# Performance work log

Hardware: AMD Instinct MI355X
Metric: run time of the kernel (lower is better)

## Reference

```python
import jax, jax.numpy as jnp
import numpy as np

NUM_GROUPS = 32
EPS = 1e-5
HEADS = 8
DIM_HEAD = 64


def group_norm(x, w, b):
    # x: [B, C, L]; normalize over (C/G, L) per group
    B, C, L = x.shape
    xg = x.reshape(B, NUM_GROUPS, C // NUM_GROUPS, L)
    mu = jnp.mean(xg, axis=(2, 3), keepdims=True)
    var = jnp.var(xg, axis=(2, 3), keepdims=True)
    xn = ((xg - mu) * jax.lax.rsqrt(var + EPS)).reshape(B, C, L)
    return xn * w[None, :, None] + b[None, :, None]


def setup_inputs() -> dict:
    key = jax.random.key(0)
    k1, k2, k3 = jax.random.split(key, 3)
    dim, hidden = 512, HEADS * DIM_HEAD
    B, L = 4, 2048
    x = jax.random.normal(k1, (B, dim, L), dtype=jnp.float32)
    gn_w = jnp.ones((dim,), jnp.float32)
    gn_b = jnp.zeros((dim,), jnp.float32)
    w_qkv = jax.random.normal(k2, (3 * hidden, dim), jnp.float32) * (dim ** -0.5)
    w_out = jax.random.normal(k3, (dim, hidden), jnp.float32) * (hidden ** -0.5)
    b_out = jnp.zeros((dim,), jnp.float32)
    return {"x": x, "gn_w": gn_w, "gn_b": gn_b, "w_qkv": w_qkv, "w_out": w_out, "b_out": b_out}


def reference(x, gn_w, gn_b, w_qkv, w_out, b_out):
    B, C, L = x.shape
    scale = DIM_HEAD ** -0.5
    nx = group_norm(x, gn_w, gn_b)
    # 1x1 conv == channel matmul: [3H*D, C] x [B, C, L] -> [B, 3H*D, L]
    qkv = jnp.einsum('oc,bcl->bol', w_qkv, nx)
    q, k, v = jnp.split(qkv, 3, axis=1)
    rs = lambda t: t.reshape(B, HEADS, DIM_HEAD, L)
    q, k, v = rs(q) * scale, rs(k), rs(v)
    sim = jnp.einsum('bhdi,bhdj->bhij', q, k)         # [B,H,L,L]
    attn = jax.nn.softmax(sim, axis=-1)
    out = jnp.einsum('bhij,bhdj->bhdi', attn, v)       # [B,H,D,L]
    out = out.reshape(B, HEADS * DIM_HEAD, L)
    proj = jnp.einsum('oc,bcl->bol', w_out, out) + b_out[None, :, None]
    return proj + x
```

## Files before the change

kernel.cpp:

```cpp
#include <hip/hip_runtime.h>

#define DEVI __device__ __forceinline__

typedef unsigned short u16;
typedef unsigned int u32;
typedef __attribute__((ext_vector_type(8))) __bf16 bf16x8;
typedef __attribute__((ext_vector_type(2))) __bf16 bf16x2;
typedef __attribute__((ext_vector_type(4))) float f32x4;
typedef __attribute__((ext_vector_type(16))) float f32x16;
typedef __attribute__((ext_vector_type(4))) u32 u32x4;

DEVI u16 f2bf(float f){
  u32 u = __float_as_uint(f);
  return (u16)((u + 0x7FFFu + ((u >> 16) & 1u)) >> 16);
}
DEVI u32 pk2(float lo, float hi){
  bf16x2 t; t[0] = (__bf16)lo; t[1] = (__bf16)hi;
  return __builtin_bit_cast(u32, t);
}

__global__ __launch_bounds__(256) void gnstat_kernel(const float* __restrict__ x,
                                                     float2* __restrict__ pstat){
  int bg = blockIdx.x >> 2, qt = blockIdx.x & 3;
  const float4* xin = (const float4*)(x + (size_t)bg*32768 + qt*8192);
  int tid = threadIdx.x;
  float s1 = 0.f, s2 = 0.f;
  #pragma unroll
  for (int i = 0; i < 8; ++i){
    float4 v = xin[tid + i*256];
    s1 += v.x + v.y + v.z + v.w;
    s2 += v.x*v.x + v.y*v.y + v.z*v.z + v.w*v.w;
  }
  __shared__ float red[8];
  int lane = tid & 63, w = tid >> 6;
  for (int off = 32; off; off >>= 1){
    s1 += __shfl_down(s1, off);
    s2 += __shfl_down(s2, off);
  }
  if (lane == 0){ red[w] = s1; red[4 + w] = s2; }
  __syncthreads();
  if (tid == 0){
    pstat[blockIdx.x] = make_float2(red[0]+red[1]+red[2]+red[3],
                                    red[4]+red[5]+red[6]+red[7]);
  }
}

__global__ __launch_bounds__(128) void gnfin_kernel(const float2* __restrict__ pstat,
                                                    float2* __restrict__ stat){
  int t = threadIdx.x;
  float s1 = 0.f, s2 = 0.f;
  #pragma unroll
  for (int i = 0; i < 4; ++i){
    float2 p = pstat[t*4 + i];
    s1 += p.x; s2 += p.y;
  }
  float mu = s1 * (1.f/32768.f);
  float var = s2 * (1.f/32768.f) - mu*mu;
  stat[t] = make_float2(mu, rsqrtf(var + 1e-5f));
}

__global__ __launch_bounds__(256) void normtrans_kernel(const float* __restrict__ x,
                                                        const float2* __restrict__ stat,
                                                        const float* __restrict__ gw,
                                                        const float* __restrict__ gb,
                                                        u16* __restrict__ nxT){
  int b = blockIdx.z, c0 = blockIdx.y * 64, l0 = blockIdx.x * 64;
  __shared__ u16 T[64][72];
  int tid = threadIdx.x;
  #pragma unroll
  for (int rep = 0; rep < 2; ++rep){
    int task = tid + rep*256;
    int r = task >> 3, cc = task & 7;
    int ch = c0 + r;
    float2 st = stat[b*32 + (ch >> 4)];
    float ga = gw[ch] * st.y;
    float be = gb[ch] - st.x * ga;
    const float4* src = (const float4*)(x + ((size_t)(b*512 + ch))*2048 + l0 + cc*8);
    float4 v0 = src[0], v1 = src[1];
    ushort4 o0, o1;
    o0.x = f2bf(v0.x*ga + be); o0.y = f2bf(v0.y*ga + be);
    o0.z = f2bf(v0.z*ga + be); o0.w = f2bf(v0.w*ga + be);
    o1.x = f2bf(v1.x*ga + be); o1.y = f2bf(v1.y*ga + be);
    o1.z = f2bf(v1.z*ga + be); o1.w = f2bf(v1.w*ga + be);
    *(ushort4*)&T[r][cc*8]     = o0;
    *(ushort4*)&T[r][cc*8 + 4] = o1;
  }
  __syncthreads();
  #pragma unroll
  for (int rep = 0; rep < 2; ++rep){
    int task = tid + rep*256;
    int r = task >> 3, cc = task & 7;
    u16 tmp[8];
    #pragma unroll
    for (int i = 0; i < 8; ++i) tmp[i] = T[cc*8 + i][r];
    *(uint4*)(nxT + ((size_t)(b*2048 + l0 + r))*512 + c0 + cc*8) = *(uint4*)tmp;
  }
}

__global__ __launch_bounds__(256) void castw_kernel(const float* __restrict__ wq,
                                                    const float* __restrict__ wo,
                                                    u16* __restrict__ wqb,
                                                    u16* __restrict__ wob){
  int t = blockIdx.x * 256 + threadIdx.x;
  const int NQ4 = (1536*512)/4;
  float4 v; u16* dst;
  if (t < NQ4){ v = ((const float4*)wq)[t]; dst = wqb + t*4; }
  else        { int u_ = t - NQ4; v = ((const float4*)wo)[u_]; dst = wob + u_*4; }
  ushort4 s;
  s.x = f2bf(v.x); s.y = f2bf(v.y); s.z = f2bf(v.z); s.w = f2bf(v.w);
  *(ushort4*)dst = s;
}

template<int MODE>
__global__ __launch_bounds__(256) void gemm_kernel(const u16* __restrict__ A,
                                                   const u16* __restrict__ Bm,
                                                   u16* __restrict__ q_o,
                                                   u16* __restrict__ k_o,
                                                   u16* __restrict__ v_o,
                                                   const float* __restrict__ bo,
                                                   const float* __restrict__ xres,
                                                   float* __restrict__ out){
  int b  = blockIdx.z;
  int n0 = blockIdx.x * 128, m0 = blockIdx.y * 128;
  int tid = threadIdx.x, w = tid >> 6, lane = tid & 63, lq = lane >> 4, lr = lane & 15;
  int wm = (w >> 1) * 64, wn = (w & 1) * 64;
  __shared__ u16 Al[2][128][40], Bl[2][128][40];
  f32x4 acc[4][4] = {};
  const u16* Bb = Bm + (size_t)b * 2048 * 512;

  for (int k0 = 0; k0 < 512; k0 += 64){
    #pragma unroll
    for (int rep = 0; rep < 4; ++rep){
      int task = tid + rep*256;
      int row = task >> 3, kc = task & 7;
      *(uint4*)&Al[kc>>2][row][(kc&3)*8] = *(const uint4*)(A  + (size_t)(m0+row)*512 + k0 + kc*8);
      *(uint4*)&Bl[kc>>2][row][(kc&3)*8] = *(const uint4*)(Bb + (size_t)(n0+row)*512 + k0 + kc*8);
    }
    __syncthreads();
    #pragma unroll
    for (int half = 0; half < 2; ++half){
      bf16x8 af[4], bfr[4];
      #pragma unroll
      for (int i = 0; i < 4; ++i) af[i]  = *(const bf16x8*)&Al[half][wm + i*16 + lr][lq*8];
      #pragma unroll
      for (int j = 0; j < 4; ++j) bfr[j] = *(const bf16x8*)&Bl[half][wn + j*16 + lr][lq*8];
      #pragma unroll
      for (int i = 0; i < 4; ++i)
        #pragma unroll
        for (int j = 0; j < 4; ++j)
          acc[i][j] = __builtin_amdgcn_mfma_f32_16x16x32_bf16(af[i], bfr[j], acc[i][j], 0, 0, 0);
    }
    __syncthreads();
  }

  if (MODE == 0){
    const float QSCALE = 0.125f * 1.4426950408889634f;
    #pragma unroll
    for (int i = 0; i < 4; ++i){
      int o0  = m0 + wm + i*16 + lq*4;
      int cls = o0 >> 9;
      int hh  = (o0 >> 6) & 7;
      int d0  = o0 & 63;
      size_t hbase = (size_t)(b*8+hh) * 2048 * 64;
      #pragma unroll
      for (int j = 0; j < 4; ++j){
        int l = n0 + wn + j*16 + lr;
        f32x4 v = acc[i][j];
        if (cls == 0){
          ushort4 s;
          s.x = f2bf(v[0]*QSCALE); s.y = f2bf(v[1]*QSCALE);
          s.z = f2bf(v[2]*QSCALE); s.w = f2bf(v[3]*QSCALE);
          *(ushort4*)(q_o + hbase + (size_t)l*64 + d0) = s;
        } else if (cls == 1){
          size_t off = (size_t)(((l>>5)*4 + (d0>>4)))*512
                     + ((d0>>3)&1)*256 + (l&31)*8 + (d0&7);
          ushort4 s;
          s.x = f2bf(v[0]); s.y = f2bf(v[1]); s.z = f2bf(v[2]); s.w = f2bf(v[3]);
          *(ushort4*)(k_o + hbase + off) = s;
        } else {
          size_t off = (size_t)(((l>>4)*2 + (d0>>5)))*512
                     + ((l>>3)&1)*256 + (l&7);
          #pragma unroll
          for (int r = 0; r < 4; ++r)
            v_o[hbase + off + ((d0+r)&31)*8] = f2bf(v[r]);
        }
      }
    }
  } else {
    #pragma unroll
    for (int i = 0; i < 4; ++i){
      int o0 = m0 + wm + i*16 + lq*4;
      #pragma unroll
      for (int j = 0; j < 4; ++j){
        int l = n0 + wn + j*16 + lr;
        #pragma unroll
        for (int r = 0; r < 4; ++r){
          int o = o0 + r;
          size_t idx = ((size_t)b*512 + o)*2048 + l;
          out[idx] = acc[i][j][r] + bo[o] + xres[idx];
        }
      }
    }
  }
}

__global__ __launch_bounds__(256, 2) void attn_kernel(const u16* __restrict__ qT,
                                                      const u16* __restrict__ kF,
                                                      const u16* __restrict__ vF,
                                                      u16* __restrict__ ao){
  int flat = blockIdx.x;
  int xcd = flat & 7, tt = flat >> 3;
  int bh = xcd*4 + (tt & 3);
  int qb = tt >> 2;
  int tid = threadIdx.x, w = tid >> 6, l = tid & 63;
  int l31 = l & 31, h = l >> 5;
  int q0 = qb*128 + w*32;
  size_t hoff = (size_t)bh * 2048 * 64;

  const u16* qp = qT + hoff + (size_t)(q0 + l31)*64 + 8*h;
  bf16x8 qf0 = *(const bf16x8*)(qp);
  bf16x8 qf1 = *(const bf16x8*)(qp + 16);
  bf16x8 qf2 = *(const bf16x8*)(qp + 32);
  bf16x8 qf3 = *(const bf16x8*)(qp + 48);

  const u16* kbase = kF + hoff + (size_t)l*8;
  const u16* vbase = vF + hoff + (size_t)l*8;

  f32x16 o0 = {}, o1 = {};
  float m = -1e30f, lsum = 0.f;

  bf16x8 kA0,kA1,kA2,kA3, kB0,kB1,kB2,kB3;
  bf16x8 vA0,vA1,vA2,vA3, vB0,vB1,vB2,vB3;
  f32x16 sA, sB;
  bf16x8 Bf0, Bf1;

#define LDK(P, t) { const u16* kt_ = kbase + (t)*2048;                         \
    P##0 = *(const bf16x8*)(kt_);        P##1 = *(const bf16x8*)(kt_ + 512);   \
    P##2 = *(const bf16x8*)(kt_ + 1024); P##3 = *(const bf16x8*)(kt_ + 1536); }
#define LDV(P, t) { const u16* vt_ = vbase + (t)*2048;                         \
    P##0 = *(const bf16x8*)(vt_);        P##1 = *(const bf16x8*)(vt_ + 512);   \
    P##2 = *(const bf16x8*)(vt_ + 1024); P##3 = *(const bf16x8*)(vt_ + 1536); }
#define QKT(S, P) {                                                            \
    S = (f32x16){};                                                            \
    __builtin_amdgcn_s_setprio(1);                                             \
    S = __builtin_amdgcn_mfma_f32_32x32x16_bf16(P##0, qf0, S, 0, 0, 0);        \
    S = __builtin_amdgcn_mfma_f32_32x32x16_bf16(P##1, qf1, S, 0, 0, 0);        \
    S = __builtin_amdgcn_mfma_f32_32x32x16_bf16(P##2, qf2, S, 0, 0, 0);        \
    S = __builtin_amdgcn_mfma_f32_32x32x16_bf16(P##3, qf3, S, 0, 0, 0);        \
    __builtin_amdgcn_s_setprio(0); }
#define SMAX(S) { \
    float c0 = fmaxf(S[0],S[1]),  c1 = fmaxf(S[2],S[3]);                       \
    float c2 = fmaxf(S[4],S[5]),  c3 = fmaxf(S[6],S[7]);                       \
    float c4 = fmaxf(S[8],S[9]),  c5 = fmaxf(S[10],S[11]);                     \
    float c6 = fmaxf(S[12],S[13]),c7 = fmaxf(S[14],S[15]);                     \
    c0 = fmaxf(c0,c1); c2 = fmaxf(c2,c3); c4 = fmaxf(c4,c5); c6 = fmaxf(c6,c7);\
    c0 = fmaxf(c0,c2); c4 = fmaxf(c4,c6); c0 = fmaxf(c0,c4);                   \
    c0 = fmaxf(c0, __shfl_xor(c0, 32));                                        \
    if (__any(c0 > m + 8.f)){                                                  \
      float nm = fmaxf(m, c0);                                                 \
      float alpha = __builtin_amdgcn_exp2f(m - nm);                            \
      m = nm; lsum *= alpha;                                                   \
      _Pragma("unroll")                                                        \
      for (int i = 0; i < 16; ++i){ o0[i] *= alpha; o1[i] *= alpha; }          \
    }                                                                          \
    float p[16];                                                               \
    _Pragma("unroll")                                                          \
    for (int i = 0; i < 16; ++i) p[i] = __builtin_amdgcn_exp2f(S[i] - m);      \
    float t0 = p[0]+p[1],  t1 = p[2]+p[3],  t2 = p[4]+p[5],  t3 = p[6]+p[7];   \
    float t4 = p[8]+p[9],  t5 = p[10]+p[11],t6 = p[12]+p[13],t7 = p[14]+p[15]; \
    t0 += t1; t2 += t3; t4 += t5; t6 += t7; t0 += t2; t4 += t6; t0 += t4;      \
    lsum += t0 + __shfl_xor(t0, 32);                                           \
    u32 a0 = pk2(p[0],p[1]),   a1 = pk2(p[2],p[3]);                            \
    u32 a2 = pk2(p[4],p[5]),   a3 = pk2(p[6],p[7]);                            \
    u32 a4 = pk2(p[8],p[9]),   a5 = pk2(p[10],p[11]);                          \
    u32 a6 = pk2(p[12],p[13]), a7 = pk2(p[14],p[15]);                          \
    u32 x0 = __shfl_xor((int)a0,32), x1 = __shfl_xor((int)a1,32);              \
    u32 x2 = __shfl_xor((int)a2,32), x3 = __shfl_xor((int)a3,32);              \
    u32 x4 = __shfl_xor((int)a4,32), x5 = __shfl_xor((int)a5,32);              \
    u32 x6 = __shfl_xor((int)a6,32), x7 = __shfl_xor((int)a7,32);              \
    u32x4 wb0, wb1;                                                            \
    wb0[0] = h ? x2 : a0;  wb0[1] = h ? x3 : a1;                               \
    wb0[2] = h ? a2 : x0;  wb0[3] = h ? a3 : x1;                               \
    wb1[0] = h ? x6 : a4;  wb1[1] = h ? x7 : a5;                               \
    wb1[2] = h ? a6 : x4;  wb1[3] = h ? a7 : x5;                               \
    Bf0 = __builtin_bit_cast(bf16x8, wb0);                                     \
    Bf1 = __builtin_bit_cast(bf16x8, wb1); }
#define PVA(P) {                                                               \
    __builtin_amdgcn_s_setprio(1);                                             \
    o0 = __builtin_amdgcn_mfma_f32_32x32x16_bf16(P##0, Bf0, o0, 0, 0, 0);      \
    o1 = __builtin_amdgcn_mfma_f32_32x32x16_bf16(P##1, Bf0, o1, 0, 0, 0);      \
    o0 = __builtin_amdgcn_mfma_f32_32x32x16_bf16(P##2, Bf1, o0, 0, 0, 0);      \
    o1 = __builtin_amdgcn_mfma_f32_32x32x16_bf16(P##3, Bf1, o1, 0, 0, 0);      \
    __builtin_amdgcn_s_setprio(0); }

  LDK(kA, 0);
  QKT(sA, kA);
  LDK(kB, 1);
  LDV(vA, 0);
  LDV(vB, 1);

  for (int t = 0; t < 64; t += 2){
    int t2 = (t+2 < 64) ? t+2 : 63;
    int t3 = (t+3 < 64) ? t+3 : 63;
    QKT(sB, kB);
    LDK(kA, t2);
    SMAX(sA);
    PVA(vA);
    LDV(vA, t2);
    QKT(sA, kA);
    LDK(kB, t3);
    SMAX(sB);
    PVA(vB);
    LDV(vB, t3);
  }

#undef LDK
#undef LDV
#undef QKT
#undef SMAX
#undef PVA

  float inv = 1.f / lsum;
  int b_ = bh >> 3, hh = bh & 7;
  size_t obase = ((size_t)(b_*2048) + q0 + l31)*512 + hh*64 + 4*h;
  #pragma unroll
  for (int s4 = 0; s4 < 4; ++s4){
    ushort4 st;
    st.x = f2bf(o0[s4*4+0]*inv); st.y = f2bf(o0[s4*4+1]*inv);
    st.z = f2bf(o0[s4*4+2]*inv); st.w = f2bf(o0[s4*4+3]*inv);
    *(ushort4*)(ao + obase + s4*8) = st;
  }
  #pragma unroll
  for (int s4 = 0; s4 < 4; ++s4){
    ushort4 st;
    st.x = f2bf(o1[s4*4+0]*inv); st.y = f2bf(o1[s4*4+1]*inv);
    st.z = f2bf(o1[s4*4+2]*inv); st.w = f2bf(o1[s4*4+3]*inv);
    *(ushort4*)(ao + obase + 32 + s4*8) = st;
  }
}

extern "C" void kernel_launch(void* const* d_in, const int* in_sizes, int n_in,
                              void* d_out, int out_size, void* d_ws, size_t ws_size,
                              hipStream_t stream) {
  const float* x    = (const float*)d_in[0];
  const float* gw   = (const float*)d_in[1];
  const float* gb   = (const float*)d_in[2];
  const float* wqkv = (const float*)d_in[3];
  const float* wout = (const float*)d_in[4];
  const float* bout = (const float*)d_in[5];
  float* out = (float*)d_out;
  char* ws = (char*)d_ws;

  const size_t MB8 = (size_t)4*512*2048*2;
  u16* ao  = (u16*)(ws);
  u16* nxT = (u16*)(ws + MB8);
  u16* wqb = (u16*)(ws + 2*MB8);
  u16* wob = (u16*)(ws + 2*MB8 + 1572864);
  u16* qT  = (u16*)(ws + 2*MB8 + 2097152);
  u16* kF  = qT + (size_t)4*8*2048*64;
  u16* vF  = kF + (size_t)4*8*2048*64;
  float2* pstat = (float2*)qT;
  float2* stat  = (float2*)((char*)qT + 8192);

  gnstat_kernel<<<512, 256, 0, stream>>>(x, pstat);
  gnfin_kernel<<<1, 128, 0, stream>>>(pstat, stat);
  castw_kernel<<<1024, 256, 0, stream>>>(wqkv, wout, wqb, wob);
  normtrans_kernel<<<dim3(32, 8, 4), 256, 0, stream>>>(x, stat, gw, gb, nxT);
  gemm_kernel<0><<<dim3(16, 12, 4), 256, 0, stream>>>(wqb, nxT, qT, kF, vF,
                                                      nullptr, nullptr, nullptr);
  attn_kernel<<<512, 256, 0, stream>>>(qT, kF, vF, ao);
  gemm_kernel<1><<<dim3(16, 4, 4), 256, 0, stream>>>(wob, ao, nullptr, nullptr, nullptr,
                                                     bout, x, out);
}
```

Baseline: 177.8 us.

## Split attention keys across wave pairs and fuse GroupNorm stats with weight cast

```diff
diff --git a/kernel.cpp b/kernel.cpp
--- a/kernel.cpp
+++ b/kernel.cpp
@@ -19,48 +19,49 @@
   return __builtin_bit_cast(u32, t);
 }
 
-__global__ __launch_bounds__(256) void gnstat_kernel(const float* __restrict__ x,
-                                                     float2* __restrict__ pstat){
-  int bg = blockIdx.x >> 2, qt = blockIdx.x & 3;
-  const float4* xin = (const float4*)(x + (size_t)bg*32768 + qt*8192);
-  int tid = threadIdx.x;
-  float s1 = 0.f, s2 = 0.f;
-  #pragma unroll
-  for (int i = 0; i < 8; ++i){
-    float4 v = xin[tid + i*256];
-    s1 += v.x + v.y + v.z + v.w;
-    s2 += v.x*v.x + v.y*v.y + v.z*v.z + v.w*v.w;
-  }
-  __shared__ float red[8];
-  int lane = tid & 63, w = tid >> 6;
-  for (int off = 32; off; off >>= 1){
-    s1 += __shfl_down(s1, off);
-    s2 += __shfl_down(s2, off);
-  }
-  if (lane == 0){ red[w] = s1; red[4 + w] = s2; }
-  __syncthreads();
-  if (tid == 0){
-    pstat[blockIdx.x] = make_float2(red[0]+red[1]+red[2]+red[3],
-                                    red[4]+red[5]+red[6]+red[7]);
-  }
-}
-
-__global__ __launch_bounds__(128) void gnfin_kernel(const float2* __restrict__ pstat,
-                                                    float2* __restrict__ stat){
-  int t = threadIdx.x;
-  float s1 = 0.f, s2 = 0.f;
-  #pragma unroll
-  for (int i = 0; i < 4; ++i){
-    float2 p = pstat[t*4 + i];
-    s1 += p.x; s2 += p.y;
-  }
-  float mu = s1 * (1.f/32768.f);
-  float var = s2 * (1.f/32768.f) - mu*mu;
-  stat[t] = make_float2(mu, rsqrtf(var + 1e-5f));
+__global__ __launch_bounds__(256) void pre_kernel(const float* __restrict__ x,
+                                                  float2* __restrict__ pstat,
+                                                  const float* __restrict__ wq,
+                                                  const float* __restrict__ wo,
+                                                  u16* __restrict__ wqb,
+                                                  u16* __restrict__ wob){
+  int bid = blockIdx.x, tid = threadIdx.x;
+  if (bid < 512){
+    int bg = bid >> 2, qt = bid & 3;
+    const float4* xin = (const float4*)(x + (size_t)bg*32768 + qt*8192);
+    float s1 = 0.f, s2 = 0.f;
+    #pragma unroll
+    for (int i = 0; i < 8; ++i){
+      float4 v = xin[tid + i*256];
+      s1 += v.x + v.y + v.z + v.w;
+      s2 += v.x*v.x + v.y*v.y + v.z*v.z + v.w*v.w;
+    }
+    __shared__ float red[8];
+    int lane = tid & 63, w = tid >> 6;
+    for (int off = 32; off; off >>= 1){
+      s1 += __shfl_down(s1, off);
+      s2 += __shfl_down(s2, off);
+    }
+    if (lane == 0){ red[w] = s1; red[4 + w] = s2; }
+    __syncthreads();
+    if (tid == 0){
+      pstat[bid] = make_float2(red[0]+red[1]+red[2]+red[3],
+                               red[4]+red[5]+red[6]+red[7]);
+    }
+  } else {
+    int t = (bid - 512) * 256 + tid;
+    const int NQ4 = (1536*512)/4;
+    float4 v; u16* dst;
+    if (t < NQ4){ v = ((const float4*)wq)[t]; dst = wqb + t*4; }
+    else        { int u_ = t - NQ4; v = ((const float4*)wo)[u_]; dst = wob + u_*4; }
+    ushort4 s;
+    s.x = f2bf(v.x); s.y = f2bf(v.y); s.z = f2bf(v.z); s.w = f2bf(v.w);
+    *(ushort4*)dst = s;
+  }
 }
 
 __global__ __launch_bounds__(256) void normtrans_kernel(const float* __restrict__ x,
-                                                        const float2* __restrict__ stat,
+                                                        const float2* __restrict__ pstat,
                                                         const float* __restrict__ gw,
                                                         const float* __restrict__ gb,
                                                         u16* __restrict__ nxT){
@@ -72,9 +73,17 @@
     int task = tid + rep*256;
     int r = task >> 3, cc = task & 7;
     int ch = c0 + r;
-    float2 st = stat[b*32 + (ch >> 4)];
-    float ga = gw[ch] * st.y;
-    float be = gb[ch] - st.x * ga;
+    int bg = b*32 + (ch >> 4);
+    float s1 = 0.f, s2 = 0.f;
+    #pragma unroll
+    for (int i = 0; i < 4; ++i){
+      float2 p = pstat[bg*4 + i];
+      s1 += p.x; s2 += p.y;
+    }
+    float mu = s1 * (1.f/32768.f);
+    float rsg = rsqrtf(s2 * (1.f/32768.f) - mu*mu + 1e-5f);
+    float ga = gw[ch] * rsg;
+    float be = gb[ch] - mu * ga;
     const float4* src = (const float4*)(x + ((size_t)(b*512 + ch))*2048 + l0 + cc*8);
     float4 v0 = src[0], v1 = src[1];
     ushort4 o0, o1;
@@ -95,20 +104,6 @@
     for (int i = 0; i < 8; ++i) tmp[i] = T[cc*8 + i][r];
     *(uint4*)(nxT + ((size_t)(b*2048 + l0 + r))*512 + c0 + cc*8) = *(uint4*)tmp;
   }
-}
-
-__global__ __launch_bounds__(256) void castw_kernel(const float* __restrict__ wq,
-                                                    const float* __restrict__ wo,
-                                                    u16* __restrict__ wqb,
-                                                    u16* __restrict__ wob){
-  int t = blockIdx.x * 256 + threadIdx.x;
-  const int NQ4 = (1536*512)/4;
-  float4 v; u16* dst;
-  if (t < NQ4){ v = ((const float4*)wq)[t]; dst = wqb + t*4; }
-  else        { int u_ = t - NQ4; v = ((const float4*)wo)[u_]; dst = wob + u_*4; }
-  ushort4 s;
-  s.x = f2bf(v.x); s.y = f2bf(v.y); s.z = f2bf(v.z); s.w = f2bf(v.w);
-  *(ushort4*)dst = s;
 }
 
 template<int MODE>
@@ -204,24 +199,26 @@
   }
 }
 
-__global__ __launch_bounds__(256, 2) void attn_kernel(const u16* __restrict__ qT,
+__global__ __launch_bounds__(256, 4) void attn_kernel(const u16* __restrict__ qT,
                                                       const u16* __restrict__ kF,
                                                       const u16* __restrict__ vF,
                                                       u16* __restrict__ ao){
   int flat = blockIdx.x;
   int xcd = flat & 7, tt = flat >> 3;
   int bh = xcd*4 + (tt & 3);
-  int qb = tt >> 2;
+  int qp = tt >> 2;
   int tid = threadIdx.x, w = tid >> 6, l = tid & 63;
   int l31 = l & 31, h = l >> 5;
-  int q0 = qb*128 + w*32;
+  int qg = w >> 1, kh = w & 1;
+  int q0 = qp*64 + qg*32;
   size_t hoff = (size_t)bh * 2048 * 64;
-
-  const u16* qp = qT + hoff + (size_t)(q0 + l31)*64 + 8*h;
-  bf16x8 qf0 = *(const bf16x8*)(qp);
-  bf16x8 qf1 = *(const bf16x8*)(qp + 16);
-  bf16x8 qf2 = *(const bf16x8*)(qp + 32);
-  bf16x8 qf3 = *(const bf16x8*)(qp + 48);
+  __shared__ float smrg[2][64][40];
+
+  const u16* qp_ = qT + hoff + (size_t)(q0 + l31)*64 + 8*h;
+  bf16x8 qf0 = *(const bf16x8*)(qp_);
+  bf16x8 qf1 = *(const bf16x8*)(qp_ + 16);
+  bf16x8 qf2 = *(const bf16x8*)(qp_ + 32);
+  bf16x8 qf3 = *(const bf16x8*)(qp_ + 48);
 
   const u16* kbase = kF + hoff + (size_t)l*8;
   const u16* vbase = vF + hoff + (size_t)l*8;
@@ -293,15 +290,16 @@
     o1 = __builtin_amdgcn_mfma_f32_32x32x16_bf16(P##3, Bf1, o1, 0, 0, 0);      \
     __builtin_amdgcn_s_setprio(0); }
 
-  LDK(kA, 0);
+  int tstart = kh*32, tend = tstart + 32;
+  LDK(kA, tstart);
   QKT(sA, kA);
-  LDK(kB, 1);
-  LDV(vA, 0);
-  LDV(vB, 1);
-
-  for (int t = 0; t < 64; t += 2){
-    int t2 = (t+2 < 64) ? t+2 : 63;
-    int t3 = (t+3 < 64) ? t+3 : 63;
+  LDK(kB, tstart+1);
+  LDV(vA, tstart);
+  LDV(vB, tstart+1);
+
+  for (int t = tstart; t < tend; t += 2){
+    int t2 = (t+2 < tend) ? t+2 : tend-1;
+    int t3 = (t+3 < tend) ? t+3 : tend-1;
     QKT(sB, kB);
     LDK(kA, t2);
     SMAX(sA);
@@ -320,22 +318,46 @@
 #undef SMAX
 #undef PVA
 
-  float inv = 1.f / lsum;
-  int b_ = bh >> 3, hh = bh & 7;
-  size_t obase = ((size_t)(b_*2048) + q0 + l31)*512 + hh*64 + 4*h;
-  #pragma unroll
-  for (int s4 = 0; s4 < 4; ++s4){
-    ushort4 st;
-    st.x = f2bf(o0[s4*4+0]*inv); st.y = f2bf(o0[s4*4+1]*inv);
-    st.z = f2bf(o0[s4*4+2]*inv); st.w = f2bf(o0[s4*4+3]*inv);
-    *(ushort4*)(ao + obase + s4*8) = st;
-  }
-  #pragma unroll
-  for (int s4 = 0; s4 < 4; ++s4){
-    ushort4 st;
-    st.x = f2bf(o1[s4*4+0]*inv); st.y = f2bf(o1[s4*4+1]*inv);
-    st.z = f2bf(o1[s4*4+2]*inv); st.w = f2bf(o1[s4*4+3]*inv);
-    *(ushort4*)(ao + obase + 32 + s4*8) = st;
+  int slot = w >> 1;
+  if (kh){
+    #pragma unroll
+    for (int j = 0; j < 4; ++j){
+      *(float4*)&smrg[slot][l][j*4]      = make_float4(o0[j*4+0], o0[j*4+1], o0[j*4+2], o0[j*4+3]);
+      *(float4*)&smrg[slot][l][16 + j*4] = make_float4(o1[j*4+0], o1[j*4+1], o1[j*4+2], o1[j*4+3]);
+    }
+    smrg[slot][l][32] = m;
+    smrg[slot][l][33] = lsum;
+  }
+  __syncthreads();
+  if (!kh){
+    float mb = smrg[slot][l][32], lb = smrg[slot][l][33];
+    float M  = fmaxf(m, mb);
+    float aA = __builtin_amdgcn_exp2f(m  - M);
+    float aB = __builtin_amdgcn_exp2f(mb - M);
+    float inv = 1.f / (lsum*aA + lb*aB);
+    float cA = aA*inv, cB = aB*inv;
+    int b_ = bh >> 3, hh = bh & 7;
+    size_t obase = ((size_t)(b_*2048) + q0 + l31)*512 + hh*64 + 4*h;
+    #pragma unroll
+    for (int s4 = 0; s4 < 4; ++s4){
+      float4 ob = *(float4*)&smrg[slot][l][s4*4];
+      ushort4 st;
+      st.x = f2bf(o0[s4*4+0]*cA + ob.x*cB);
+      st.y = f2bf(o0[s4*4+1]*cA + ob.y*cB);
+      st.z = f2bf(o0[s4*4+2]*cA + ob.z*cB);
+      st.w = f2bf(o0[s4*4+3]*cA + ob.w*cB);
+      *(ushort4*)(ao + obase + s4*8) = st;
+    }
+    #pragma unroll
+    for (int s4 = 0; s4 < 4; ++s4){
+      float4 ob = *(float4*)&smrg[slot][l][16 + s4*4];
+      ushort4 st;
+      st.x = f2bf(o1[s4*4+0]*cA + ob.x*cB);
+      st.y = f2bf(o1[s4*4+1]*cA + ob.y*cB);
+      st.z = f2bf(o1[s4*4+2]*cA + ob.z*cB);
+      st.w = f2bf(o1[s4*4+3]*cA + ob.w*cB);
+      *(ushort4*)(ao + obase + 32 + s4*8) = st;
+    }
   }
 }
 
@@ -360,15 +382,12 @@
   u16* kF  = qT + (size_t)4*8*2048*64;
   u16* vF  = kF + (size_t)4*8*2048*64;
   float2* pstat = (float2*)qT;
-  float2* stat  = (float2*)((char*)qT + 8192);
-
-  gnstat_kernel<<<512, 256, 0, stream>>>(x, pstat);
-  gnfin_kernel<<<1, 128, 0, stream>>>(pstat, stat);
-  castw_kernel<<<1024, 256, 0, stream>>>(wqkv, wout, wqb, wob);
-  normtrans_kernel<<<dim3(32, 8, 4), 256, 0, stream>>>(x, stat, gw, gb, nxT);
+
+  pre_kernel<<<1536, 256, 0, stream>>>(x, pstat, wqkv, wout, wqb, wob);
+  normtrans_kernel<<<dim3(32, 8, 4), 256, 0, stream>>>(x, pstat, gw, gb, nxT);
   gemm_kernel<0><<<dim3(16, 12, 4), 256, 0, stream>>>(wqb, nxT, qT, kF, vF,
                                                       nullptr, nullptr, nullptr);
-  attn_kernel<<<512, 256, 0, stream>>>(qT, kF, vF, ao);
+  attn_kernel<<<1024, 256, 0, stream>>>(qT, kF, vF, ao);
   gemm_kernel<1><<<dim3(16, 4, 4), 256, 0, stream>>>(wob, ao, nullptr, nullptr, nullptr,
                                                      bout, x, out);
 }
```

After: 248.8 us. 40.0% more time.
